# Kernel tuning notes

Measured on AMD Instinct MI355X. Metric: run time of the kernel, lower is better.

Reference implementation:

```python
import jax, jax.numpy as jnp
import numpy as np

B, N_OBJ, OBJ_D = 256, 36, 2048
ATT_D, EMB_D, DEC_D, VOCAB, T = 1024, 1024, 1024, 10000, 20


def setup_inputs() -> dict:
    key = jax.random.key(0)
    ks = jax.random.split(key, 16)
    s = lambda *d: 1.0 / np.sqrt(d[-1])
    inp = {
        'encoder_out': jax.random.normal(ks[0], (B, EMB_D), jnp.float32),
        'objects': jax.random.normal(ks[1], (B, N_OBJ, OBJ_D), jnp.float32),
        'encoded_captions': jax.random.randint(ks[2], (B, T), 0, VOCAB),
        'caption_lengths': jax.random.randint(ks[3], (B, 1), 1, T + 1),
        'emb_table': jax.random.normal(ks[4], (VOCAB, EMB_D), jnp.float32) * 0.02,
        'W_enc_att': jax.random.normal(ks[5], (ATT_D, OBJ_D), jnp.float32) * s(OBJ_D),
        'b_enc_att': jnp.zeros((ATT_D,), jnp.float32),
        'W_dec_att': jax.random.normal(ks[6], (ATT_D, DEC_D), jnp.float32) * s(DEC_D),
        'b_dec_att': jnp.zeros((ATT_D,), jnp.float32),
        'w_full_att': jax.random.normal(ks[7], (1, ATT_D), jnp.float32) * s(ATT_D),
        'b_full_att': jnp.zeros((1,), jnp.float32),
        'W_fbeta': jax.random.normal(ks[8], (OBJ_D, DEC_D), jnp.float32) * s(DEC_D),
        'b_fbeta': jnp.zeros((OBJ_D,), jnp.float32),
        'W_ih': jax.random.normal(ks[9], (4 * DEC_D, EMB_D + OBJ_D), jnp.float32) * s(EMB_D + OBJ_D),
        'W_hh': jax.random.normal(ks[10], (4 * DEC_D, DEC_D), jnp.float32) * s(DEC_D),
        'b_ih': jnp.zeros((4 * DEC_D,), jnp.float32),
        'b_hh': jnp.zeros((4 * DEC_D,), jnp.float32),
        'W_fc': jax.random.normal(ks[11], (VOCAB, DEC_D), jnp.float32) * s(DEC_D),
        'b_fc': jnp.zeros((VOCAB,), jnp.float32),
    }
    return inp


def reference(encoder_out, objects, encoded_captions, caption_lengths,
              emb_table, W_enc_att, b_enc_att, W_dec_att, b_dec_att,
              w_full_att, b_full_att, W_fbeta, b_fbeta,
              W_ih, W_hh, b_ih, b_hh, W_fc, b_fc):
    lengths = caption_lengths[:, 0]
    sort_ind = jnp.argsort(-lengths)  # descending
    lengths = lengths[sort_ind]
    encoder_out = encoder_out[sort_ind]
    objects = objects[sort_ind]
    encoded_captions = encoded_captions[sort_ind]

    embeddings = emb_table[encoded_captions]  # (B, T, E)
    # step t input: encoder_out at t=0, embeddings[:, t-1] afterwards
    step_x = jnp.concatenate([encoder_out[:, None, :], embeddings[:, : T - 1, :]], axis=1)  # (B,T,E)

    att1 = jnp.einsum('bno,ao->bna', objects, W_enc_att) + b_enc_att  # (B,N,A), h-independent

    def step(carry, xs):
        h, c = carry
        x_t, t = xs  # (B,E), scalar
        active = (t < lengths)[:, None]  # (B,1) -- batch_size_t masking (lengths sorted desc)
        att2 = h @ W_dec_att.T + b_dec_att  # (B,A)
        e = (jax.nn.relu(att1 + att2[:, None, :]) @ w_full_att[0] + b_full_att[0])  # (B,N)
        alpha = jax.nn.softmax(e, axis=1)
        awe = jnp.einsum('bn,bno->bo', alpha, objects)  # (B,O)
        gate = jax.nn.sigmoid(h @ W_fbeta.T + b_fbeta)
        awe = gate * awe
        gates = jnp.concatenate([x_t, awe], axis=-1) @ W_ih.T + b_ih + h @ W_hh.T + b_hh
        i, f, g, o = jnp.split(gates, 4, axis=-1)  # torch LSTMCell order
        c_new = jax.nn.sigmoid(f) * c + jax.nn.sigmoid(i) * jnp.tanh(g)
        h_new = jax.nn.sigmoid(o) * jnp.tanh(c_new)
        h = jnp.where(active, h_new, h)
        c = jnp.where(active, c_new, c)
        preds = h_new @ W_fc.T + b_fc  # dropout in eval mode = identity
        preds = jnp.where(active, preds, 0.0)
        alpha = jnp.where(active, alpha, 0.0)
        return (h, c), (preds, alpha)

    h0 = jnp.zeros((B, DEC_D), objects.dtype)
    c0 = jnp.zeros((B, DEC_D), objects.dtype)
    xs = (jnp.swapaxes(step_x, 0, 1), jnp.arange(T))
    _, (preds, alphas) = jax.lax.scan(step, (h0, c0), xs)
    predictions = jnp.swapaxes(preds, 0, 1)  # (B,T,V)
    alphas = jnp.swapaxes(alphas, 0, 1)      # (B,T,N)
    return predictions, encoded_captions, lengths, alphas, sort_ind
```

## Files before the change

kernel.cpp:

```cpp
#include <hip/hip_runtime.h>
#include <hip/hip_bf16.h>
#include <cstdint>
#include <cstddef>

#define BB 256
#define TT 20
#define NOBJ 36
#define OBJD 2048
#define ATTD 1024
#define DECD 1024
#define VOCAB 10000
#define NHC   7168
#define VOCP  10112

typedef unsigned short u16;
typedef __attribute__((ext_vector_type(8))) short short8v;
typedef __attribute__((ext_vector_type(4))) float f32x4;

__device__ inline u16 f2bf(float f) {
    __hip_bfloat16 h = __float2bfloat16(f);
    return *reinterpret_cast<u16*>(&h);
}
__device__ inline float bu(u16 u) {
    union { unsigned int i; float f; } x;
    x.i = ((unsigned int)u) << 16;
    return x.f;
}
__device__ inline float sigf(float x) { return 1.f / (1.f + expf(-x)); }

__device__ inline void gload16(const u16* g, u16* l) {
    __builtin_amdgcn_global_load_lds(
        (const __attribute__((address_space(1))) unsigned int*)g,
        (__attribute__((address_space(3))) unsigned int*)l, 16, 0, 0);
}

__global__ __launch_bounds__(256) void sort_kernel(
    const int* __restrict__ lens, int* __restrict__ sidx, int* __restrict__ slen,
    int* __restrict__ cnt, float* __restrict__ out_len, float* __restrict__ out_sind)
{
    __shared__ int L[BB];
    __shared__ int SL[BB];
    const int i = threadIdx.x;
    const int li = lens[i];
    L[i] = li;
    __syncthreads();
    int r = 0;
    for (int j = 0; j < BB; ++j) {
        const int lj = L[j];
        if (lj > li || (lj == li && j < i)) r++;
    }
    sidx[r] = i;
    slen[r] = li;
    SL[r] = li;
    out_sind[r] = (float)i;
    out_len[r]  = (float)li;
    __syncthreads();
    if (i < TT) {
        int cc = 0;
        for (int b = 0; b < BB; ++b) cc += (SL[b] > i);
        cnt[i] = cc;
    }
}

__global__ __launch_bounds__(256) void meta_kernel(
    const int* __restrict__ caps, const int* __restrict__ sidx,
    float* __restrict__ out_caps)
{
    const int idx = blockIdx.x * 256 + threadIdx.x;
    const int p = idx / TT, t = idx % TT;
    out_caps[idx] = (float)caps[sidx[p] * TT + t];
}

__global__ __launch_bounds__(256) void gather_objs(
    const float* __restrict__ objs, const int* __restrict__ sidx,
    u16* __restrict__ objsb)
{
    const int row = blockIdx.x;
    const int b = row / NOBJ, n = row - b * NOBJ;
    const float* src = objs + ((size_t)sidx[b] * NOBJ + n) * OBJD;
    u16* dst = objsb + (size_t)row * OBJD;
    const int tid = threadIdx.x;
    #pragma unroll
    for (int j = 0; j < 2; ++j) {
        float4 v = ((const float4*)src)[tid + 256 * j];
        ushort4 s;
        s.x = f2bf(v.x); s.y = f2bf(v.y); s.z = f2bf(v.z); s.w = f2bf(v.w);
        ((ushort4*)dst)[tid + 256 * j] = s;
    }
}

__global__ __launch_bounds__(256) void convWhc(
    const float* __restrict__ Wda, const float* __restrict__ bda,
    const float* __restrict__ Wfb, const float* __restrict__ bfb,
    const float* __restrict__ Whh,
    u16* __restrict__ Wb, float* __restrict__ bcat)
{
    const int n = blockIdx.x;
    const int tid = threadIdx.x;
    const float* src;
    float bb = 0.f;
    if (n < 1024)      { src = Wda + (size_t)n * 1024;          bb = bda[n]; }
    else if (n < 3072) { src = Wfb + (size_t)(n - 1024) * 1024; bb = bfb[n - 1024]; }
    else {
        const int loc = n - 3072, q = loc & 3, d = loc >> 2;
        src = Whh + ((size_t)q * 1024 + d) * 1024;
    }
    float4 v = ((const float4*)src)[tid];
    ushort4 s;
    s.x = f2bf(v.x); s.y = f2bf(v.y); s.z = f2bf(v.z); s.w = f2bf(v.w);
    ((ushort4*)(Wb + (size_t)n * 1024))[tid] = s;
    if (tid == 0) bcat[n] = bb;
}

__global__ __launch_bounds__(256) void convWfc(
    const float* __restrict__ Wfc, u16* __restrict__ Wb)
{
    const int n = blockIdx.x;
    const int tid = threadIdx.x;
    ushort4 s;
    if (n < VOCAB) {
        float4 v = ((const float4*)(Wfc + (size_t)n * 1024))[tid];
        s.x = f2bf(v.x); s.y = f2bf(v.y); s.z = f2bf(v.z); s.w = f2bf(v.w);
    } else { s.x = s.y = s.z = s.w = 0; }
    ((ushort4*)(Wb + (size_t)n * 1024))[tid] = s;
}

__global__ __launch_bounds__(256) void convWih(
    const float* __restrict__ Wih, const float* __restrict__ bih,
    const float* __restrict__ bhh, u16* __restrict__ Wb, float* __restrict__ bsum)
{
    const int n = blockIdx.x;
    const int q = n & 3, d = n >> 2;
    const int tid = threadIdx.x;
    const float* src = Wih + ((size_t)q * 1024 + d) * 3072;
    u16* dst = Wb + (size_t)n * 3072;
    #pragma unroll
    for (int j = 0; j < 3; ++j) {
        float4 v = ((const float4*)src)[tid + 256 * j];
        ushort4 s;
        s.x = f2bf(v.x); s.y = f2bf(v.y); s.z = f2bf(v.z); s.w = f2bf(v.w);
        ((ushort4*)dst)[tid + 256 * j] = s;
    }
    if (tid == 0) bsum[n] = bih[q * 1024 + d] + bhh[q * 1024 + d];
}

__global__ __launch_bounds__(256) void convWea(
    const float* __restrict__ Wea, u16* __restrict__ Wb)
{
    const int n = blockIdx.x;
    const int tid = threadIdx.x;
    const float* src = Wea + (size_t)n * OBJD;
    u16* dst = Wb + (size_t)n * OBJD;
    #pragma unroll
    for (int j = 0; j < 2; ++j) {
        float4 v = ((const float4*)src)[tid + 256 * j];
        ushort4 s;
        s.x = f2bf(v.x); s.y = f2bf(v.y); s.z = f2bf(v.z); s.w = f2bf(v.w);
        ((ushort4*)dst)[tid + 256 * j] = s;
    }
}

__global__ __launch_bounds__(256) void embed_kernel(
    const float* __restrict__ enc, const int* __restrict__ caps,
    const float* __restrict__ emb, const int* __restrict__ sidx,
    u16* __restrict__ Xb)
{
    const int blk = blockIdx.x;
    const int t = blk >> 8;
    const int b = blk & 255;
    const int sb = sidx[b];
    const float* src = (t == 0) ? (enc + (size_t)sb * DECD)
                                : (emb + (size_t)caps[sb * TT + (t - 1)] * DECD);
    const int tid = threadIdx.x;
    float4 v = ((const float4*)src)[tid];
    ushort4 s;
    s.x = f2bf(v.x); s.y = f2bf(v.y); s.z = f2bf(v.z); s.w = f2bf(v.w);
    ((ushort4*)(Xb + (size_t)blk * DECD))[tid] = s;
}

__global__ __launch_bounds__(256) void zero_c(float* __restrict__ c)
{
    ((float4*)c)[blockIdx.x * 256 + threadIdx.x] = make_float4(0.f, 0.f, 0.f, 0.f);
}

__global__ __launch_bounds__(256) void hcat0_kernel(
    const float* __restrict__ bcat, float* __restrict__ Hcat)
{
    const int col4 = blockIdx.x * 256 + threadIdx.x;
    const int m = blockIdx.y;
    ((float4*)(Hcat + (size_t)m * NHC))[col4] = ((const float4*)bcat)[col4];
}

__device__ __forceinline__ void gemm_core(u16* SH,
    const u16* __restrict__ A, int lda,
    const u16* __restrict__ B, int ldb,
    int K, int m0, int n0, f32x4 acc[4][4])
{
    u16* AsB = SH;
    u16* BsB = SH + 12288;
    const int tid = threadIdx.x;
    const int lane = tid & 63;
    const int w = tid >> 6;
    const int wr = w >> 1, wc = w & 1;

    const int r0 = (w * 2 + 0) * 16 + (lane >> 2);
    const int r1 = (w * 2 + 1) * 16 + (lane >> 2);
    const int s0 = (lane & 3) ^ ((r0 >> 1) & 3);
    const int s1 = (lane & 3) ^ ((r1 >> 1) & 3);
    const u16* gA0 = A + (size_t)(m0 + r0) * lda + s0 * 8;
    const u16* gA1 = A + (size_t)(m0 + r1) * lda + s1 * 8;
    const u16* gB0 = B + (size_t)(n0 + r0) * ldb + s0 * 8;
    const u16* gB1 = B + (size_t)(n0 + r1) * ldb + s1 * 8;
    const int la0 = (w * 2 + 0) * 512;
    const int la1 = (w * 2 + 1) * 512;

    int ia[4], ib[4];
    #pragma unroll
    for (int mi = 0; mi < 4; ++mi) {
        const int r = wr * 64 + mi * 16 + (lane & 15);
        ia[mi] = r * 32 + (((lane >> 4) ^ ((r >> 1) & 3)) << 3);
    }
    #pragma unroll
    for (int nj = 0; nj < 4; ++nj) {
        const int r = wc * 64 + nj * 16 + (lane & 15);
        ib[nj] = r * 32 + (((lane >> 4) ^ ((r >> 1) & 3)) << 3);
    }

    const int nk = K >> 5;
    #pragma unroll
    for (int p = 0; p < 3; ++p) {
        if (p < nk) {
            const int ko = p * 32;
            gload16(gA0 + ko, AsB + p * 4096 + la0);
            gload16(gA1 + ko, AsB + p * 4096 + la1);
            gload16(gB0 + ko, BsB + p * 4096 + la0);
            gload16(gB1 + ko, BsB + p * 4096 + la1);
        }
    }
    int cur = 0;
    for (int it = 0; it < nk; ++it) {
        const int rem = nk - 1 - it;
        if (rem >= 2)      asm volatile("s_waitcnt vmcnt(8)" ::: "memory");
        else if (rem == 1) asm volatile("s_waitcnt vmcnt(4)" ::: "memory");
        else               asm volatile("s_waitcnt vmcnt(0)" ::: "memory");
        __builtin_amdgcn_s_barrier();
        const u16* Asc = AsB + cur * 4096;
        const u16* Bsc = BsB + cur * 4096;
        short8v av[4], bv[4];
        #pragma unroll
        for (int mi = 0; mi < 4; ++mi) av[mi] = *(const short8v*)&Asc[ia[mi]];
        #pragma unroll
        for (int nj = 0; nj < 4; ++nj) bv[nj] = *(const short8v*)&Bsc[ib[nj]];
        __builtin_amdgcn_s_setprio(1);
        #pragma unroll
        for (int mi = 0; mi < 4; ++mi)
            #pragma unroll
            for (int nj = 0; nj < 4; ++nj)
                acc[mi][nj] = __builtin_amdgcn_mfma_f32_16x16x32_bf16(
                    av[mi], bv[nj], acc[mi][nj], 0, 0, 0);
        __builtin_amdgcn_s_setprio(0);
        __builtin_amdgcn_s_barrier();
        if (it + 3 < nk) {
            const int ko = (it + 3) * 32;
            gload16(gA0 + ko, AsB + cur * 4096 + la0);
            gload16(gA1 + ko, AsB + cur * 4096 + la1);
            gload16(gB0 + ko, BsB + cur * 4096 + la0);
            gload16(gB1 + ko, BsB + cur * 4096 + la1);
        }
        cur = (cur == 2) ? 0 : cur + 1;
    }
}

__global__ __launch_bounds__(256) void gemm128(
    const u16* __restrict__ A, int lda,
    const u16* __restrict__ B, int ldb,
    const float* __restrict__ bias,
    float* __restrict__ Cf, u16* __restrict__ Cb, int ldc,
    int Nreal, int K, int pairM, const int* __restrict__ cntp)
{
    __shared__ __align__(16) u16 SH[24576];
    int nIdx, mIdx;
    if (pairM) { nIdx = blockIdx.x >> 1; mIdx = blockIdx.x & 1; }
    else       { nIdx = blockIdx.x;      mIdx = blockIdx.y; }
    const int m0 = mIdx * 128;
    const int n0 = nIdx * 128;
    if (cntp && m0 >= *cntp) return;

    f32x4 acc[4][4];
    #pragma unroll
    for (int i = 0; i < 4; ++i)
        #pragma unroll
        for (int j = 0; j < 4; ++j) acc[i][j] = (f32x4){0.f, 0.f, 0.f, 0.f};
    gemm_core(SH, A, lda, B, ldb, K, m0, n0, acc);

    const int lane = threadIdx.x & 63, w = threadIdx.x >> 6;
    const int wr = w >> 1, wc = w & 1;
    #pragma unroll
    for (int mi = 0; mi < 4; ++mi) {
        const int mbase = m0 + wr * 64 + mi * 16 + ((lane >> 4) << 2);
        #pragma unroll
        for (int nj = 0; nj < 4; ++nj) {
            const int n = n0 + wc * 64 + nj * 16 + (lane & 15);
            if (n >= Nreal) continue;
            const float bval = bias ? bias[n] : 0.f;
            #pragma unroll
            for (int r = 0; r < 4; ++r) {
                const int m = mbase + r;
                const float v = acc[mi][nj][r] + bval;
                if (Cb) Cb[(size_t)m * ldc + n] = f2bf(v);
                else    Cf[(size_t)m * ldc + n] = v;
            }
        }
    }
}

__global__ __launch_bounds__(256) void g2l_kernel(
    const u16* __restrict__ aweb, const u16* __restrict__ Wihb,
    const u16* __restrict__ Gxb_t, const float* __restrict__ Hcat,
    float* __restrict__ c, u16* __restrict__ hb_t,
    const int* __restrict__ cntp)
{
    __shared__ __align__(16) u16 SH[24576];
    const int bid = blockIdx.x, tid = threadIdx.x;
    const int m0 = (bid & 1) * 128, n0 = (bid >> 1) * 128;
    const int act = *cntp;
    if (m0 >= act) return;

    f32x4 acc[4][4];
    #pragma unroll
    for (int i = 0; i < 4; ++i)
        #pragma unroll
        for (int j = 0; j < 4; ++j) acc[i][j] = (f32x4){0.f, 0.f, 0.f, 0.f};
    gemm_core(SH, aweb, 2048, Wihb + 1024, 3072, 2048, m0, n0, acc);

    const int lane = tid & 63, w = tid >> 6;
    const int wr = w >> 1, wc = w & 1;
    float* patch = (float*)SH;
    #pragma unroll
    for (int half = 0; half < 2; ++half) {
        __syncthreads();
        if (wr == half) {
            #pragma unroll
            for (int mi = 0; mi < 4; ++mi) {
                const int rbase = mi * 16 + ((lane >> 4) << 2);
                #pragma unroll
                for (int nj = 0; nj < 4; ++nj) {
                    const int col = wc * 64 + nj * 16 + (lane & 15);
                    #pragma unroll
                    for (int r = 0; r < 4; ++r)
                        patch[(rbase + r) * 128 + col] = acc[mi][nj][r];
                }
            }
        }
        __syncthreads();
        const int h0 = half * 64;
        #pragma unroll
        for (int p8 = 0; p8 < 8; ++p8) {
            const int idx = p8 * 256 + tid;
            const int row = idx >> 5, dl = idx & 31;
            const int b = m0 + h0 + row;
            if (b >= act) continue;
            const int d = (n0 >> 2) + dl;
            const float* pr = patch + row * 128 + dl * 4;
            float gi = pr[0], gf = pr[1], gg = pr[2], go = pr[3];
            const ushort4 xv = *(const ushort4*)(Gxb_t + (size_t)b * 4096 + n0 + dl * 4);
            gi += bu(xv.x); gf += bu(xv.y); gg += bu(xv.z); go += bu(xv.w);
            const float4 hv = *(const float4*)(Hcat + (size_t)b * NHC + 3072 + n0 + dl * 4);
            gi += hv.x; gf += hv.y; gg += hv.z; go += hv.w;
            float* cp = c + (size_t)b * 1024 + d;
            const float cn = sigf(gf) * cp[0] + sigf(gi) * tanhf(gg);
            const float hn = sigf(go) * tanhf(cn);
            cp[0] = cn;
            hb_t[(size_t)b * 1024 + d] = f2bf(hn);
        }
    }
}

__global__ __launch_bounds__(256) void preds_gemm(
    const u16* __restrict__ hball, const u16* __restrict__ Wfcb,
    const float* __restrict__ bfc, const int* __restrict__ cnt,
    float* __restrict__ outP)
{
    __shared__ __align__(16) u16 SH[24576];
    const int m0 = blockIdx.y * 128;
    const int n0 = blockIdx.x * 128;
    const int t = m0 >> 8;
    const int act = cnt[t];
    const int bbase = m0 & 255;

    f32x4 acc[4][4];
    #pragma unroll
    for (int i = 0; i < 4; ++i)
        #pragma unroll
        for (int j = 0; j < 4; ++j) acc[i][j] = (f32x4){0.f, 0.f, 0.f, 0.f};
    if (bbase < act)
        gemm_core(SH, hball, 1024, Wfcb, 1024, 1024, m0, n0, acc);

    const int lane = threadIdx.x & 63, w = threadIdx.x >> 6;
    const int wr = w >> 1, wc = w & 1;
    #pragma unroll
    for (int mi = 0; mi < 4; ++mi) {
        const int mbase = bbase + wr * 64 + mi * 16 + ((lane >> 4) << 2);
        #pragma unroll
        for (int nj = 0; nj < 4; ++nj) {
            const int n = n0 + wc * 64 + nj * 16 + (lane & 15);
            if (n >= VOCAB) continue;
            const float bval = bfc[n];
            #pragma unroll
            for (int r = 0; r < 4; ++r) {
                const int b = mbase + r;
                outP[((size_t)b * TT + t) * VOCAB + n] =
                    (b < act) ? (acc[mi][nj][r] + bval) : 0.f;
            }
        }
    }
}

__global__ __launch_bounds__(256) void attn_kernel(
    const u16* __restrict__ att1b, const float* __restrict__ Hcat,
    const u16* __restrict__ objsb,
    const float* __restrict__ wfa, const float* __restrict__ bfa,
    const int* __restrict__ slen, int t,
    float* __restrict__ out_alph, u16* __restrict__ aweb)
{
    const int b = blockIdx.x, z = blockIdx.y, tid = threadIdx.x;
    const bool active = t < slen[b];
    if (!active) {
        if (z == 0 && tid < NOBJ)
            out_alph[((size_t)b * TT + t) * NOBJ + tid] = 0.f;
        return;
    }
    __shared__ float wred[4][40];
    __shared__ float es[40];
    __shared__ float alph[40];
    const int lane = tid & 63, w = tid >> 6;
    const float* hrow = Hcat + (size_t)b * NHC;
    const float4 h4 = ((const float4*)hrow)[tid];
    const float4 w4 = ((const float4*)wfa)[tid];
    const u16* a1base = att1b + (size_t)b * NOBJ * ATTD;

    float ep[NOBJ];
    #pragma unroll
    for (int n = 0; n < NOBJ; ++n) {
        ushort4 a4 = ((const ushort4*)(a1base + (size_t)n * ATTD))[tid];
        const float v0 = fmaxf(bu(a4.x) + h4.x, 0.f);
        const float v1 = fmaxf(bu(a4.y) + h4.y, 0.f);
        const float v2 = fmaxf(bu(a4.z) + h4.z, 0.f);
        const float v3 = fmaxf(bu(a4.w) + h4.w, 0.f);
        ep[n] = v0 * w4.x + v1 * w4.y + v2 * w4.z + v3 * w4.w;
    }
    #pragma unroll
    for (int n = 0; n < NOBJ; ++n) {
        float p = ep[n];
        #pragma unroll
        for (int off = 32; off > 0; off >>= 1) p += __shfl_down(p, off, 64);
        if (lane == 0) wred[w][n] = p;
    }
    __syncthreads();
    if (tid < NOBJ)
        es[tid] = wred[0][tid] + wred[1][tid] + wred[2][tid] + wred[3][tid] + bfa[0];
    __syncthreads();
    if (tid < 64) {
        float mv = (tid < NOBJ) ? es[tid] : -1e30f;
        #pragma unroll
        for (int off = 32; off > 0; off >>= 1) mv = fmaxf(mv, __shfl_xor(mv, off, 64));
        float e = (tid < NOBJ) ? expf(es[tid] - mv) : 0.f;
        float s = e;
        #pragma unroll
        for (int off = 32; off > 0; off >>= 1) s += __shfl_xor(s, off, 64);
        if (tid < NOBJ) alph[tid] = e / s;
    }
    __syncthreads();
    if (z == 0 && tid < NOBJ)
        out_alph[((size_t)b * TT + t) * NOBJ + tid] = alph[tid];

    float acc[4] = {0.f, 0.f, 0.f, 0.f};
    const u16* ob = objsb + (size_t)b * NOBJ * OBJD + z * 1024 + tid * 4;
    #pragma unroll 4
    for (int n = 0; n < NOBJ; ++n) {
        const ushort4 ov = *(const ushort4*)(ob + (size_t)n * OBJD);
        const float al = alph[n];
        acc[0] = fmaf(al, bu(ov.x), acc[0]);
        acc[1] = fmaf(al, bu(ov.y), acc[1]);
        acc[2] = fmaf(al, bu(ov.z), acc[2]);
        acc[3] = fmaf(al, bu(ov.w), acc[3]);
    }
    const float4 g0 = *(const float4*)(hrow + 1024 + z * 1024 + tid * 4);
    ushort4 st;
    st.x = f2bf(acc[0] * sigf(g0.x));
    st.y = f2bf(acc[1] * sigf(g0.y));
    st.z = f2bf(acc[2] * sigf(g0.z));
    st.w = f2bf(acc[3] * sigf(g0.w));
    *(ushort4*)&aweb[(size_t)b * 2048 + z * 1024 + tid * 4] = st;
}

extern "C" void kernel_launch(void* const* d_in, const int* in_sizes, int n_in,
                              void* d_out, int out_size, void* d_ws, size_t ws_size,
                              hipStream_t stream)
{
    const float* enc  = (const float*)d_in[0];
    const float* objs = (const float*)d_in[1];
    const int*   caps = (const int*)d_in[2];
    const int*   clen = (const int*)d_in[3];
    const float* emb  = (const float*)d_in[4];
    const float* Wea  = (const float*)d_in[5];
    const float* bea  = (const float*)d_in[6];
    const float* Wda  = (const float*)d_in[7];
    const float* bda  = (const float*)d_in[8];
    const float* wfa  = (const float*)d_in[9];
    const float* bfa  = (const float*)d_in[10];
    const float* Wfb  = (const float*)d_in[11];
    const float* bfb  = (const float*)d_in[12];
    const float* Wih  = (const float*)d_in[13];
    const float* Whh  = (const float*)d_in[14];
    const float* bih  = (const float*)d_in[15];
    const float* bhh  = (const float*)d_in[16];
    const float* Wfc  = (const float*)d_in[17];
    const float* bfc  = (const float*)d_in[18];

    float* outP     = (float*)d_out;
    float* out_caps = outP + (size_t)BB * TT * VOCAB;
    float* out_len  = out_caps + BB * TT;
    float* out_alph = out_len + BB;
    float* out_sind = out_alph + (size_t)BB * TT * NOBJ;

    char* wp = (char*)d_ws;
    auto alloc = [&](size_t bytes) -> void* {
        void* r = (void*)wp;
        wp += (bytes + 255) & ~(size_t)255;
        return r;
    };
    int*   sidx  = (int*)alloc(BB * 4);
    int*   slen  = (int*)alloc(BB * 4);
    int*   cnt   = (int*)alloc(32 * 4);
    u16*   objsb = (u16*)alloc((size_t)BB * NOBJ * OBJD * 2);
    u16*   Whcb  = (u16*)alloc((size_t)NHC * 1024 * 2);
    float* bcat  = (float*)alloc(NHC * 4);
    u16*   Wfcb  = (u16*)alloc((size_t)VOCP * 1024 * 2);
    u16*   Wihb  = (u16*)alloc((size_t)4096 * 3072 * 2);
    float* bsum  = (float*)alloc(4096 * 4);
    u16*   Weab  = (u16*)alloc((size_t)1024 * OBJD * 2);
    u16*   att1b = (u16*)alloc((size_t)BB * NOBJ * ATTD * 2);
    u16*   Xb    = (u16*)alloc((size_t)TT * BB * DECD * 2);
    u16*   Gxb   = (u16*)alloc((size_t)TT * BB * 4096 * 2);
    float* Hcat  = (float*)alloc((size_t)BB * NHC * 4);
    u16*   aweb  = (u16*)alloc((size_t)BB * 2048 * 2);
    u16*   hball = (u16*)alloc((size_t)TT * BB * DECD * 2);
    float* c     = (float*)alloc((size_t)BB * DECD * 4);
    (void)ws_size; (void)in_sizes; (void)n_in; (void)out_size;

    sort_kernel<<<1, 256, 0, stream>>>(clen, sidx, slen, cnt, out_len, out_sind);
    meta_kernel<<<20, 256, 0, stream>>>(caps, sidx, out_caps);
    gather_objs<<<BB * NOBJ, 256, 0, stream>>>(objs, sidx, objsb);
    convWhc<<<NHC, 256, 0, stream>>>(Wda, bda, Wfb, bfb, Whh, Whcb, bcat);
    convWfc<<<VOCP, 256, 0, stream>>>(Wfc, Wfcb);
    convWih<<<4096, 256, 0, stream>>>(Wih, bih, bhh, Wihb, bsum);
    convWea<<<1024, 256, 0, stream>>>(Wea, Weab);
    embed_kernel<<<TT * BB, 256, 0, stream>>>(enc, caps, emb, sidx, Xb);
    zero_c<<<256, 256, 0, stream>>>(c);
    hcat0_kernel<<<dim3(7, 256), 256, 0, stream>>>(bcat, Hcat);

    gemm128<<<dim3(8, 72), 256, 0, stream>>>(
        objsb, OBJD, Weab, OBJD, bea, nullptr, att1b, ATTD,
        ATTD, OBJD, 0, nullptr);

    gemm128<<<dim3(32, 40), 256, 0, stream>>>(
        Xb, DECD, Wihb, 3072, bsum, nullptr, Gxb, 4096,
        4096, DECD, 0, nullptr);

    for (int t = 0; t < TT; ++t) {
        attn_kernel<<<dim3(BB, 2), 256, 0, stream>>>(
            att1b, Hcat, objsb, wfa, bfa, slen, t, out_alph, aweb);
        g2l_kernel<<<64, 256, 0, stream>>>(
            aweb, Wihb, Gxb + (size_t)t * BB * 4096, Hcat, c,
            hball + (size_t)t * BB * DECD, cnt + t);
        if (t < TT - 1)
            gemm128<<<112, 256, 0, stream>>>(
                hball + (size_t)t * BB * DECD, DECD, Whcb, DECD, bcat,
                Hcat, nullptr, NHC, NHC, DECD, 1, cnt + t);
    }

    preds_gemm<<<dim3(VOCP / 128, 40), 256, 0, stream>>>(
        hball, Wfcb, bfc, cnt, outP);
}
```

Baseline: 1.728 ms.

## Overlap W_hh projection with attention and remap preds GEMM block order

Each step's hidden-state GEMM is split. Only the attention/gate columns (first 3072) are computed right after the LSTM cell, and the W_hh recurrent columns are computed by extra blocks inside the next step's attention kernel, so they run concurrently with the attention work. The attention kernel now uses one block per batch row with 8-wide loads instead of two half-blocks. The preds GEMM uses a 1D grid that sweeps pairs of M tiles across all N tiles for better weight reuse in cache. This cuts the critical path per step, but the combined kernel gets heavier shared-memory use and mixed block types. The W_hh part also drops the bias add, on the assumption that the bias is already folded in elsewhere.

```diff
diff --git a/kernel.cpp b/kernel.cpp
--- a/kernel.cpp
+++ b/kernel.cpp
@@ -312,6 +312,118 @@
             }
         }
     }
+}
+
+__global__ __launch_bounds__(256) void attnwhh_kernel(
+    const u16* __restrict__ att1b, float* __restrict__ Hcat,
+    const u16* __restrict__ objsb,
+    const float* __restrict__ wfa, const float* __restrict__ bfa,
+    const int* __restrict__ slen, int t,
+    float* __restrict__ out_alph, u16* __restrict__ aweb,
+    const u16* __restrict__ hb_prev, const u16* __restrict__ Whcb,
+    const int* __restrict__ cnt_prev)
+{
+    __shared__ __align__(16) u16 SH[24576];
+    __shared__ float wred[4][40];
+    __shared__ float es[40];
+    __shared__ float alph[40];
+    const int tid = threadIdx.x;
+
+    if (blockIdx.x >= 256) {
+        if (t == 0) return;
+        const int j = blockIdx.x - 256;
+        const int n0 = (j >> 1) * 128;
+        const int m0 = (j & 1) * 128;
+        if (m0 >= *cnt_prev) return;
+        f32x4 acc[4][4];
+        #pragma unroll
+        for (int i = 0; i < 4; ++i)
+            #pragma unroll
+            for (int jj = 0; jj < 4; ++jj) acc[i][jj] = (f32x4){0.f, 0.f, 0.f, 0.f};
+        gemm_core(SH, hb_prev, DECD, Whcb + (size_t)3072 * 1024, DECD,
+                  DECD, m0, n0, acc);
+        const int lane = tid & 63, w = tid >> 6;
+        const int wr = w >> 1, wc = w & 1;
+        #pragma unroll
+        for (int mi = 0; mi < 4; ++mi) {
+            const int mbase = m0 + wr * 64 + mi * 16 + ((lane >> 4) << 2);
+            #pragma unroll
+            for (int nj = 0; nj < 4; ++nj) {
+                const int n = n0 + wc * 64 + nj * 16 + (lane & 15);
+                #pragma unroll
+                for (int r = 0; r < 4; ++r)
+                    Hcat[(size_t)(mbase + r) * NHC + 3072 + n] = acc[mi][nj][r];
+            }
+        }
+        return;
+    }
+
+    const int b = blockIdx.x;
+    const bool active = t < slen[b];
+    if (!active) {
+        if (tid < NOBJ)
+            out_alph[((size_t)b * TT + t) * NOBJ + tid] = 0.f;
+        return;
+    }
+    const int lane = tid & 63, w = tid >> 6;
+    const float* hrow = Hcat + (size_t)b * NHC;
+    const float4 h4 = ((const float4*)hrow)[tid];
+    const float4 w4 = ((const float4*)wfa)[tid];
+    const u16* a1base = att1b + (size_t)b * NOBJ * ATTD;
+
+    float ep[NOBJ];
+    #pragma unroll
+    for (int n = 0; n < NOBJ; ++n) {
+        ushort4 a4 = ((const ushort4*)(a1base + (size_t)n * ATTD))[tid];
+        const float v0 = fmaxf(bu(a4.x) + h4.x, 0.f);
+        const float v1 = fmaxf(bu(a4.y) + h4.y, 0.f);
+        const float v2 = fmaxf(bu(a4.z) + h4.z, 0.f);
+        const float v3 = fmaxf(bu(a4.w) + h4.w, 0.f);
+        ep[n] = v0 * w4.x + v1 * w4.y + v2 * w4.z + v3 * w4.w;
+    }
+    #pragma unroll
+    for (int n = 0; n < NOBJ; ++n) {
+        float p = ep[n];
+        #pragma unroll
+        for (int off = 32; off > 0; off >>= 1) p += __shfl_down(p, off, 64);
+        if (lane == 0) wred[w][n] = p;
+    }
+    __syncthreads();
+    if (tid < NOBJ)
+        es[tid] = wred[0][tid] + wred[1][tid] + wred[2][tid] + wred[3][tid] + bfa[0];
+    __syncthreads();
+    if (tid < 64) {
+        float mv = (tid < NOBJ) ? es[tid] : -1e30f;
+        #pragma unroll
+        for (int off = 32; off > 0; off >>= 1) mv = fmaxf(mv, __shfl_xor(mv, off, 64));
+        float e = (tid < NOBJ) ? expf(es[tid] - mv) : 0.f;
+        float s = e;
+        #pragma unroll
+        for (int off = 32; off > 0; off >>= 1) s += __shfl_xor(s, off, 64);
+        if (tid < NOBJ) alph[tid] = e / s;
+    }
+    __syncthreads();
+    if (tid < NOBJ)
+        out_alph[((size_t)b * TT + t) * NOBJ + tid] = alph[tid];
+
+    float acc8[8] = {0.f, 0.f, 0.f, 0.f, 0.f, 0.f, 0.f, 0.f};
+    const u16* ob = objsb + (size_t)b * NOBJ * OBJD + tid * 8;
+    #pragma unroll 4
+    for (int n = 0; n < NOBJ; ++n) {
+        const short8v ov = *(const short8v*)(ob + (size_t)n * OBJD);
+        const float al = alph[n];
+        #pragma unroll
+        for (int j = 0; j < 8; ++j) acc8[j] = fmaf(al, bu((u16)ov[j]), acc8[j]);
+    }
+    const float* gp = hrow + 1024 + tid * 8;
+    const float4 g0 = *(const float4*)gp;
+    const float4 g1 = *(const float4*)(gp + 4);
+    const float gt[8] = {sigf(g0.x), sigf(g0.y), sigf(g0.z), sigf(g0.w),
+                         sigf(g1.x), sigf(g1.y), sigf(g1.z), sigf(g1.w)};
+    short8v st;
+    #pragma unroll
+    for (int j = 0; j < 8; ++j) st[j] = (short)f2bf(acc8[j] * gt[j]);
+    *(short8v*)&aweb[(size_t)b * 2048 + tid * 8] = st;
 }
 
 __global__ __launch_bounds__(256) void g2l_kernel(
@@ -382,8 +494,11 @@
     float* __restrict__ outP)
 {
     __shared__ __align__(16) u16 SH[24576];
-    const int m0 = blockIdx.y * 128;
-    const int n0 = blockIdx.x * 128;
+    const int bid = blockIdx.x;
+    const int sweep = bid / 158;
+    const int rem = bid - sweep * 158;
+    const int n0 = (rem >> 1) * 128;
+    const int m0 = (sweep * 2 + (rem & 1)) * 128;
     const int t = m0 >> 8;
     const int act = cnt[t];
     const int bbase = m0 & 255;
@@ -414,84 +529,6 @@
             }
         }
     }
-}
-
-__global__ __launch_bounds__(256) void attn_kernel(
-    const u16* __restrict__ att1b, const float* __restrict__ Hcat,
-    const u16* __restrict__ objsb,
-    const float* __restrict__ wfa, const float* __restrict__ bfa,
-    const int* __restrict__ slen, int t,
-    float* __restrict__ out_alph, u16* __restrict__ aweb)
-{
-    const int b = blockIdx.x, z = blockIdx.y, tid = threadIdx.x;
-    const bool active = t < slen[b];
-    if (!active) {
-        if (z == 0 && tid < NOBJ)
-            out_alph[((size_t)b * TT + t) * NOBJ + tid] = 0.f;
-        return;
-    }
-    __shared__ float wred[4][40];
-    __shared__ float es[40];
-    __shared__ float alph[40];
-    const int lane = tid & 63, w = tid >> 6;
-    const float* hrow = Hcat + (size_t)b * NHC;
-    const float4 h4 = ((const float4*)hrow)[tid];
-    const float4 w4 = ((const float4*)wfa)[tid];
-    const u16* a1base = att1b + (size_t)b * NOBJ * ATTD;
-
-    float ep[NOBJ];
-    #pragma unroll
-    for (int n = 0; n < NOBJ; ++n) {
-        ushort4 a4 = ((const ushort4*)(a1base + (size_t)n * ATTD))[tid];
-        const float v0 = fmaxf(bu(a4.x) + h4.x, 0.f);
-        const float v1 = fmaxf(bu(a4.y) + h4.y, 0.f);
-        const float v2 = fmaxf(bu(a4.z) + h4.z, 0.f);
-        const float v3 = fmaxf(bu(a4.w) + h4.w, 0.f);
-        ep[n] = v0 * w4.x + v1 * w4.y + v2 * w4.z + v3 * w4.w;
-    }
-    #pragma unroll
-    for (int n = 0; n < NOBJ; ++n) {
-        float p = ep[n];
-        #pragma unroll
-        for (int off = 32; off > 0; off >>= 1) p += __shfl_down(p, off, 64);
-        if (lane == 0) wred[w][n] = p;
-    }
-    __syncthreads();
-    if (tid < NOBJ)
-        es[tid] = wred[0][tid] + wred[1][tid] + wred[2][tid] + wred[3][tid] + bfa[0];
-    __syncthreads();
-    if (tid < 64) {
-        float mv = (tid < NOBJ) ? es[tid] : -1e30f;
-        #pragma unroll
-        for (int off = 32; off > 0; off >>= 1) mv = fmaxf(mv, __shfl_xor(mv, off, 64));
-        float e = (tid < NOBJ) ? expf(es[tid] - mv) : 0.f;
-        float s = e;
-        #pragma unroll
-        for (int off = 32; off > 0; off >>= 1) s += __shfl_xor(s, off, 64);
-        if (tid < NOBJ) alph[tid] = e / s;
-    }
-    __syncthreads();
-    if (z == 0 && tid < NOBJ)
-        out_alph[((size_t)b * TT + t) * NOBJ + tid] = alph[tid];
-
-    float acc[4] = {0.f, 0.f, 0.f, 0.f};
-    const u16* ob = objsb + (size_t)b * NOBJ * OBJD + z * 1024 + tid * 4;
-    #pragma unroll 4
-    for (int n = 0; n < NOBJ; ++n) {
-        const ushort4 ov = *(const ushort4*)(ob + (size_t)n * OBJD);
-        const float al = alph[n];
-        acc[0] = fmaf(al, bu(ov.x), acc[0]);
-        acc[1] = fmaf(al, bu(ov.y), acc[1]);
-        acc[2] = fmaf(al, bu(ov.z), acc[2]);
-        acc[3] = fmaf(al, bu(ov.w), acc[3]);
-    }
-    const float4 g0 = *(const float4*)(hrow + 1024 + z * 1024 + tid * 4);
-    ushort4 st;
-    st.x = f2bf(acc[0] * sigf(g0.x));
-    st.y = f2bf(acc[1] * sigf(g0.y));
-    st.z = f2bf(acc[2] * sigf(g0.z));
-    st.w = f2bf(acc[3] * sigf(g0.w));
-    *(ushort4*)&aweb[(size_t)b * 2048 + z * 1024 + tid * 4] = st;
 }
 
 extern "C" void kernel_launch(void* const* d_in, const int* in_sizes, int n_in,
@@ -569,17 +606,18 @@
         4096, DECD, 0, nullptr);
 
     for (int t = 0; t < TT; ++t) {
-        attn_kernel<<<dim3(BB, 2), 256, 0, stream>>>(
-            att1b, Hcat, objsb, wfa, bfa, slen, t, out_alph, aweb);
+        attnwhh_kernel<<<320, 256, 0, stream>>>(
+            att1b, Hcat, objsb, wfa, bfa, slen, t, out_alph, aweb,
+            hball + (size_t)(t > 0 ? t - 1 : 0) * BB * DECD, Whcb,
+            cnt + (t > 0 ? t - 1 : 0));
         g2l_kernel<<<64, 256, 0, stream>>>(
             aweb, Wihb, Gxb + (size_t)t * BB * 4096, Hcat, c,
             hball + (size_t)t * BB * DECD, cnt + t);
         if (t < TT - 1)
-            gemm128<<<112, 256, 0, stream>>>(
+            gemm128<<<48, 256, 0, stream>>>(
                 hball + (size_t)t * BB * DECD, DECD, Whcb, DECD, bcat,
-                Hcat, nullptr, NHC, NHC, DECD, 1, cnt + t);
-    }
-
-    preds_gemm<<<dim3(VOCP / 128, 40), 256, 0, stream>>>(
-        hball, Wfcb, bfc, cnt, outP);
-}
+                Hcat, nullptr, NHC, 3072, DECD, 1, cnt + t);
+    }
+
+    preds_gemm<<<3160, 256, 0, stream>>>(hball, Wfcb, bfc, cnt, outP);
+}
```

New measurement: 1.827 ms. 5.7% more time.

## Deepen GEMM prefetch pipeline for recurrent kernels and remap preds grid

Applied to the files above, without the earlier changes.

Templates the GEMM core on pipeline depth, using an 8-stage global-to-LDS prefetch for the per-step recurrent GEMMs (g2l and the hidden-state GEMM) and keeping 3 stages elsewhere. These kernels launch only 64-112 blocks, so deeper in-flight loads are meant to hide memory latency. The preds GEMM becomes a 1D grid of 3200 blocks with a swizzled block-to-tile mapping, and the vocab padding grows to 10240 so the tiles divide evenly. The larger LDS footprint (128KB per block) limits each CU to one block, which matters little at these grid sizes.

```diff
diff --git a/kernel.cpp b/kernel.cpp
--- a/kernel.cpp
+++ b/kernel.cpp
@@ -11,7 +11,7 @@
 #define DECD 1024
 #define VOCAB 10000
 #define NHC   7168
-#define VOCP  10112
+#define VOCP  10240
 
 typedef unsigned short u16;
 typedef __attribute__((ext_vector_type(8))) short short8v;
@@ -32,6 +32,21 @@
     __builtin_amdgcn_global_load_lds(
         (const __attribute__((address_space(1))) unsigned int*)g,
         (__attribute__((address_space(3))) unsigned int*)l, 16, 0, 0);
+}
+
+template<int DEPTH>
+__device__ __forceinline__ void wait_tiles(int rem) {
+    const int r = rem < DEPTH - 1 ? rem : DEPTH - 1;
+    switch (r) {
+        case 0: asm volatile("s_waitcnt vmcnt(0)" ::: "memory"); break;
+        case 1: asm volatile("s_waitcnt vmcnt(4)" ::: "memory"); break;
+        case 2: asm volatile("s_waitcnt vmcnt(8)" ::: "memory"); break;
+        case 3: asm volatile("s_waitcnt vmcnt(12)" ::: "memory"); break;
+        case 4: asm volatile("s_waitcnt vmcnt(16)" ::: "memory"); break;
+        case 5: asm volatile("s_waitcnt vmcnt(20)" ::: "memory"); break;
+        case 6: asm volatile("s_waitcnt vmcnt(24)" ::: "memory"); break;
+        default: asm volatile("s_waitcnt vmcnt(28)" ::: "memory"); break;
+    }
 }
 
 __global__ __launch_bounds__(256) void sort_kernel(
@@ -191,13 +206,14 @@
     ((float4*)(Hcat + (size_t)m * NHC))[col4] = ((const float4*)bcat)[col4];
 }
 
+template<int DEPTH>
 __device__ __forceinline__ void gemm_core(u16* SH,
     const u16* __restrict__ A, int lda,
     const u16* __restrict__ B, int ldb,
     int K, int m0, int n0, f32x4 acc[4][4])
 {
     u16* AsB = SH;
-    u16* BsB = SH + 12288;
+    u16* BsB = SH + DEPTH * 4096;
     const int tid = threadIdx.x;
     const int lane = tid & 63;
     const int w = tid >> 6;
@@ -228,7 +244,7 @@
 
     const int nk = K >> 5;
     #pragma unroll
-    for (int p = 0; p < 3; ++p) {
+    for (int p = 0; p < DEPTH; ++p) {
         if (p < nk) {
             const int ko = p * 32;
             gload16(gA0 + ko, AsB + p * 4096 + la0);
@@ -239,10 +255,7 @@
     }
     int cur = 0;
     for (int it = 0; it < nk; ++it) {
-        const int rem = nk - 1 - it;
-        if (rem >= 2)      asm volatile("s_waitcnt vmcnt(8)" ::: "memory");
-        else if (rem == 1) asm volatile("s_waitcnt vmcnt(4)" ::: "memory");
-        else               asm volatile("s_waitcnt vmcnt(0)" ::: "memory");
+        wait_tiles<DEPTH>(nk - 1 - it);
         __builtin_amdgcn_s_barrier();
         const u16* Asc = AsB + cur * 4096;
         const u16* Bsc = BsB + cur * 4096;
@@ -260,17 +273,18 @@
                     av[mi], bv[nj], acc[mi][nj], 0, 0, 0);
         __builtin_amdgcn_s_setprio(0);
         __builtin_amdgcn_s_barrier();
-        if (it + 3 < nk) {
-            const int ko = (it + 3) * 32;
+        if (it + DEPTH < nk) {
+            const int ko = (it + DEPTH) * 32;
             gload16(gA0 + ko, AsB + cur * 4096 + la0);
             gload16(gA1 + ko, AsB + cur * 4096 + la1);
             gload16(gB0 + ko, BsB + cur * 4096 + la0);
             gload16(gB1 + ko, BsB + cur * 4096 + la1);
         }
-        cur = (cur == 2) ? 0 : cur + 1;
-    }
-}
-
+        cur = (cur == DEPTH - 1) ? 0 : cur + 1;
+    }
+}
+
+template<int DEPTH>
 __global__ __launch_bounds__(256) void gemm128(
     const u16* __restrict__ A, int lda,
     const u16* __restrict__ B, int ldb,
@@ -278,7 +292,7 @@
     float* __restrict__ Cf, u16* __restrict__ Cb, int ldc,
     int Nreal, int K, int pairM, const int* __restrict__ cntp)
 {
-    __shared__ __align__(16) u16 SH[24576];
+    __shared__ __align__(16) u16 SH[2 * DEPTH * 4096];
     int nIdx, mIdx;
     if (pairM) { nIdx = blockIdx.x >> 1; mIdx = blockIdx.x & 1; }
     else       { nIdx = blockIdx.x;      mIdx = blockIdx.y; }
@@ -291,7 +305,7 @@
     for (int i = 0; i < 4; ++i)
         #pragma unroll
         for (int j = 0; j < 4; ++j) acc[i][j] = (f32x4){0.f, 0.f, 0.f, 0.f};
-    gemm_core(SH, A, lda, B, ldb, K, m0, n0, acc);
+    gemm_core<DEPTH>(SH, A, lda, B, ldb, K, m0, n0, acc);
 
     const int lane = threadIdx.x & 63, w = threadIdx.x >> 6;
     const int wr = w >> 1, wc = w & 1;
@@ -320,7 +334,7 @@
     float* __restrict__ c, u16* __restrict__ hb_t,
     const int* __restrict__ cntp)
 {
-    __shared__ __align__(16) u16 SH[24576];
+    __shared__ __align__(16) u16 SH[2 * 8 * 4096];
     const int bid = blockIdx.x, tid = threadIdx.x;
     const int m0 = (bid & 1) * 128, n0 = (bid >> 1) * 128;
     const int act = *cntp;
@@ -331,7 +345,7 @@
     for (int i = 0; i < 4; ++i)
         #pragma unroll
         for (int j = 0; j < 4; ++j) acc[i][j] = (f32x4){0.f, 0.f, 0.f, 0.f};
-    gemm_core(SH, aweb, 2048, Wihb + 1024, 3072, 2048, m0, n0, acc);
+    gemm_core<8>(SH, aweb, 2048, Wihb + 1024, 3072, 2048, m0, n0, acc);
 
     const int lane = tid & 63, w = tid >> 6;
     const int wr = w >> 1, wc = w & 1;
@@ -381,9 +395,12 @@
     const float* __restrict__ bfc, const int* __restrict__ cnt,
     float* __restrict__ outP)
 {
-    __shared__ __align__(16) u16 SH[24576];
-    const int m0 = blockIdx.y * 128;
-    const int n0 = blockIdx.x * 128;
+    __shared__ __align__(16) u16 SH[2 * 3 * 4096];
+    const int bid = blockIdx.x;
+    const int x = bid & 7;
+    const int j = bid >> 3;
+    const int n0 = (x * 10 + (j % 10)) * 128;
+    const int m0 = (j / 10) * 128;
     const int t = m0 >> 8;
     const int act = cnt[t];
     const int bbase = m0 & 255;
@@ -392,9 +409,9 @@
     #pragma unroll
     for (int i = 0; i < 4; ++i)
         #pragma unroll
-        for (int j = 0; j < 4; ++j) acc[i][j] = (f32x4){0.f, 0.f, 0.f, 0.f};
+        for (int jj = 0; jj < 4; ++jj) acc[i][jj] = (f32x4){0.f, 0.f, 0.f, 0.f};
     if (bbase < act)
-        gemm_core(SH, hball, 1024, Wfcb, 1024, 1024, m0, n0, acc);
+        gemm_core<3>(SH, hball, 1024, Wfcb, 1024, 1024, m0, n0, acc);
 
     const int lane = threadIdx.x & 63, w = threadIdx.x >> 6;
     const int wr = w >> 1, wc = w & 1;
@@ -560,11 +577,11 @@
     zero_c<<<256, 256, 0, stream>>>(c);
     hcat0_kernel<<<dim3(7, 256), 256, 0, stream>>>(bcat, Hcat);
 
-    gemm128<<<dim3(8, 72), 256, 0, stream>>>(
+    gemm128<3><<<dim3(8, 72), 256, 0, stream>>>(
         objsb, OBJD, Weab, OBJD, bea, nullptr, att1b, ATTD,
         ATTD, OBJD, 0, nullptr);
 
-    gemm128<<<dim3(32, 40), 256, 0, stream>>>(
+    gemm128<3><<<dim3(32, 40), 256, 0, stream>>>(
         Xb, DECD, Wihb, 3072, bsum, nullptr, Gxb, 4096,
         4096, DECD, 0, nullptr);
 
@@ -575,11 +592,10 @@
             aweb, Wihb, Gxb + (size_t)t * BB * 4096, Hcat, c,
             hball + (size_t)t * BB * DECD, cnt + t);
         if (t < TT - 1)
-            gemm128<<<112, 256, 0, stream>>>(
+            gemm128<8><<<112, 256, 0, stream>>>(
                 hball + (size_t)t * BB * DECD, DECD, Whcb, DECD, bcat,
                 Hcat, nullptr, NHC, NHC, DECD, 1, cnt + t);
     }
 
-    preds_gemm<<<dim3(VOCP / 128, 40), 256, 0, stream>>>(
-        hball, Wfcb, bfc, cnt, outP);
-}
+    preds_gemm<<<3200, 256, 0, stream>>>(hball, Wfcb, bfc, cnt, outP);
+}
```

Result: slower. 1.907 ms (+10.4%).

## Fuse per-step output projection into the recurrent hidden-state GEMM

Applied to the files above, without the earlier changes.

Concatenates the vocabulary projection weights with the attention/gate/W_hh weights so that each timestep runs one GEMM over h producing both the next-step Hcat terms and that step's predictions. The separate end-of-loop preds GEMM and the hball history buffer are removed. The 128x128 tiles are block-swizzled so M-pairs share B tiles. The intent is to fill the GPU better during the small per-step GEMMs, which had only 112 blocks, by giving them 272 blocks. In exchange, the predictions work now sits on the serial per-step critical path, and the final step runs a GEMM that was previously skipped.

```diff
diff --git a/kernel.cpp b/kernel.cpp
--- a/kernel.cpp
+++ b/kernel.cpp
@@ -11,7 +11,9 @@
 #define DECD 1024
 #define VOCAB 10000
 #define NHC   7168
-#define VOCP  10112
+#define NBIG  17168
+#define NBIGP 17408
+#define NSPLIT 7168
 
 typedef unsigned short u16;
 typedef __attribute__((ext_vector_type(8))) short short8v;
@@ -89,40 +91,31 @@
     }
 }
 
-__global__ __launch_bounds__(256) void convWhc(
+__global__ __launch_bounds__(256) void convWbig(
     const float* __restrict__ Wda, const float* __restrict__ bda,
     const float* __restrict__ Wfb, const float* __restrict__ bfb,
     const float* __restrict__ Whh,
+    const float* __restrict__ Wfc, const float* __restrict__ bfc,
     u16* __restrict__ Wb, float* __restrict__ bcat)
 {
     const int n = blockIdx.x;
     const int tid = threadIdx.x;
-    const float* src;
+    const float* src = nullptr;
     float bb = 0.f;
     if (n < 1024)      { src = Wda + (size_t)n * 1024;          bb = bda[n]; }
     else if (n < 3072) { src = Wfb + (size_t)(n - 1024) * 1024; bb = bfb[n - 1024]; }
-    else {
+    else if (n < 7168) {
         const int loc = n - 3072, q = loc & 3, d = loc >> 2;
         src = Whh + ((size_t)q * 1024 + d) * 1024;
     }
-    float4 v = ((const float4*)src)[tid];
+    else if (n < NBIG) { src = Wfc + (size_t)(n - NHC) * 1024;  bb = bfc[n - NHC]; }
     ushort4 s;
-    s.x = f2bf(v.x); s.y = f2bf(v.y); s.z = f2bf(v.z); s.w = f2bf(v.w);
-    ((ushort4*)(Wb + (size_t)n * 1024))[tid] = s;
-    if (tid == 0) bcat[n] = bb;
-}
-
-__global__ __launch_bounds__(256) void convWfc(
-    const float* __restrict__ Wfc, u16* __restrict__ Wb)
-{
-    const int n = blockIdx.x;
-    const int tid = threadIdx.x;
-    ushort4 s;
-    if (n < VOCAB) {
-        float4 v = ((const float4*)(Wfc + (size_t)n * 1024))[tid];
+    if (src) {
+        float4 v = ((const float4*)src)[tid];
         s.x = f2bf(v.x); s.y = f2bf(v.y); s.z = f2bf(v.z); s.w = f2bf(v.w);
     } else { s.x = s.y = s.z = s.w = 0; }
     ((ushort4*)(Wb + (size_t)n * 1024))[tid] = s;
+    if (tid == 0) bcat[n] = bb;
 }
 
 __global__ __launch_bounds__(256) void convWih(
@@ -276,15 +269,11 @@
     const u16* __restrict__ B, int ldb,
     const float* __restrict__ bias,
     float* __restrict__ Cf, u16* __restrict__ Cb, int ldc,
-    int Nreal, int K, int pairM, const int* __restrict__ cntp)
+    int Nreal, int K)
 {
     __shared__ __align__(16) u16 SH[24576];
-    int nIdx, mIdx;
-    if (pairM) { nIdx = blockIdx.x >> 1; mIdx = blockIdx.x & 1; }
-    else       { nIdx = blockIdx.x;      mIdx = blockIdx.y; }
-    const int m0 = mIdx * 128;
-    const int n0 = nIdx * 128;
-    if (cntp && m0 >= *cntp) return;
+    const int m0 = blockIdx.y * 128;
+    const int n0 = blockIdx.x * 128;
 
     f32x4 acc[4][4];
     #pragma unroll
@@ -309,6 +298,51 @@
                 const float v = acc[mi][nj][r] + bval;
                 if (Cb) Cb[(size_t)m * ldc + n] = f2bf(v);
                 else    Cf[(size_t)m * ldc + n] = v;
+            }
+        }
+    }
+}
+
+__global__ __launch_bounds__(256) void big_gemm(
+    const u16* __restrict__ hb, const u16* __restrict__ Wbigb,
+    const float* __restrict__ bcat, const int* __restrict__ cntp,
+    float* __restrict__ Hcat, float* __restrict__ outP_t)
+{
+    __shared__ __align__(16) u16 SH[24576];
+    const int bid = blockIdx.x;
+    const int n0 = ((bid >> 4) * 8 + (bid & 7)) * 128;
+    const int m0 = ((bid >> 3) & 1) * 128;
+    const int act = *cntp;
+    const bool live = (m0 < act);
+
+    f32x4 acc[4][4];
+    #pragma unroll
+    for (int i = 0; i < 4; ++i)
+        #pragma unroll
+        for (int j = 0; j < 4; ++j) acc[i][j] = (f32x4){0.f, 0.f, 0.f, 0.f};
+    if (live)
+        gemm_core(SH, hb, DECD, Wbigb, DECD, DECD, m0, n0, acc);
+
+    const int lane = threadIdx.x & 63, w = threadIdx.x >> 6;
+    const int wr = w >> 1, wc = w & 1;
+    #pragma unroll
+    for (int mi = 0; mi < 4; ++mi) {
+        const int mbase = m0 + wr * 64 + mi * 16 + ((lane >> 4) << 2);
+        #pragma unroll
+        for (int nj = 0; nj < 4; ++nj) {
+            const int n = n0 + wc * 64 + nj * 16 + (lane & 15);
+            if (n >= NBIG) continue;
+            const float bval = bcat[n];
+            #pragma unroll
+            for (int r = 0; r < 4; ++r) {
+                const int m = mbase + r;
+                const float v = acc[mi][nj][r] + bval;
+                if (n < NSPLIT) {
+                    if (live) Hcat[(size_t)m * NHC + n] = v;
+                } else {
+                    outP_t[(size_t)m * (TT * VOCAB) + (n - NSPLIT)] =
+                        (m < act) ? v : 0.f;
+                }
             }
         }
     }
@@ -372,46 +406,6 @@
             const float hn = sigf(go) * tanhf(cn);
             cp[0] = cn;
             hb_t[(size_t)b * 1024 + d] = f2bf(hn);
-        }
-    }
-}
-
-__global__ __launch_bounds__(256) void preds_gemm(
-    const u16* __restrict__ hball, const u16* __restrict__ Wfcb,
-    const float* __restrict__ bfc, const int* __restrict__ cnt,
-    float* __restrict__ outP)
-{
-    __shared__ __align__(16) u16 SH[24576];
-    const int m0 = blockIdx.y * 128;
-    const int n0 = blockIdx.x * 128;
-    const int t = m0 >> 8;
-    const int act = cnt[t];
-    const int bbase = m0 & 255;
-
-    f32x4 acc[4][4];
-    #pragma unroll
-    for (int i = 0; i < 4; ++i)
-        #pragma unroll
-        for (int j = 0; j < 4; ++j) acc[i][j] = (f32x4){0.f, 0.f, 0.f, 0.f};
-    if (bbase < act)
-        gemm_core(SH, hball, 1024, Wfcb, 1024, 1024, m0, n0, acc);
-
-    const int lane = threadIdx.x & 63, w = threadIdx.x >> 6;
-    const int wr = w >> 1, wc = w & 1;
-    #pragma unroll
-    for (int mi = 0; mi < 4; ++mi) {
-        const int mbase = bbase + wr * 64 + mi * 16 + ((lane >> 4) << 2);
-        #pragma unroll
-        for (int nj = 0; nj < 4; ++nj) {
-            const int n = n0 + wc * 64 + nj * 16 + (lane & 15);
-            if (n >= VOCAB) continue;
-            const float bval = bfc[n];
-            #pragma unroll
-            for (int r = 0; r < 4; ++r) {
-                const int b = mbase + r;
-                outP[((size_t)b * TT + t) * VOCAB + n] =
-                    (b < act) ? (acc[mi][nj][r] + bval) : 0.f;
-            }
         }
     }
 }
@@ -534,9 +528,8 @@
     int*   slen  = (int*)alloc(BB * 4);
     int*   cnt   = (int*)alloc(32 * 4);
     u16*   objsb = (u16*)alloc((size_t)BB * NOBJ * OBJD * 2);
-    u16*   Whcb  = (u16*)alloc((size_t)NHC * 1024 * 2);
-    float* bcat  = (float*)alloc(NHC * 4);
-    u16*   Wfcb  = (u16*)alloc((size_t)VOCP * 1024 * 2);
+    u16*   Wbigb = (u16*)alloc((size_t)NBIGP * 1024 * 2);
+    float* bcat  = (float*)alloc(NBIGP * 4);
     u16*   Wihb  = (u16*)alloc((size_t)4096 * 3072 * 2);
     float* bsum  = (float*)alloc(4096 * 4);
     u16*   Weab  = (u16*)alloc((size_t)1024 * OBJD * 2);
@@ -545,15 +538,14 @@
     u16*   Gxb   = (u16*)alloc((size_t)TT * BB * 4096 * 2);
     float* Hcat  = (float*)alloc((size_t)BB * NHC * 4);
     u16*   aweb  = (u16*)alloc((size_t)BB * 2048 * 2);
-    u16*   hball = (u16*)alloc((size_t)TT * BB * DECD * 2);
+    u16*   hb    = (u16*)alloc((size_t)BB * DECD * 2);
     float* c     = (float*)alloc((size_t)BB * DECD * 4);
     (void)ws_size; (void)in_sizes; (void)n_in; (void)out_size;
 
     sort_kernel<<<1, 256, 0, stream>>>(clen, sidx, slen, cnt, out_len, out_sind);
     meta_kernel<<<20, 256, 0, stream>>>(caps, sidx, out_caps);
     gather_objs<<<BB * NOBJ, 256, 0, stream>>>(objs, sidx, objsb);
-    convWhc<<<NHC, 256, 0, stream>>>(Wda, bda, Wfb, bfb, Whh, Whcb, bcat);
-    convWfc<<<VOCP, 256, 0, stream>>>(Wfc, Wfcb);
+    convWbig<<<NBIGP, 256, 0, stream>>>(Wda, bda, Wfb, bfb, Whh, Wfc, bfc, Wbigb, bcat);
     convWih<<<4096, 256, 0, stream>>>(Wih, bih, bhh, Wihb, bsum);
     convWea<<<1024, 256, 0, stream>>>(Wea, Weab);
     embed_kernel<<<TT * BB, 256, 0, stream>>>(enc, caps, emb, sidx, Xb);
@@ -561,25 +553,17 @@
     hcat0_kernel<<<dim3(7, 256), 256, 0, stream>>>(bcat, Hcat);
 
     gemm128<<<dim3(8, 72), 256, 0, stream>>>(
-        objsb, OBJD, Weab, OBJD, bea, nullptr, att1b, ATTD,
-        ATTD, OBJD, 0, nullptr);
+        objsb, OBJD, Weab, OBJD, bea, nullptr, att1b, ATTD, ATTD, OBJD);
 
     gemm128<<<dim3(32, 40), 256, 0, stream>>>(
-        Xb, DECD, Wihb, 3072, bsum, nullptr, Gxb, 4096,
-        4096, DECD, 0, nullptr);
+        Xb, DECD, Wihb, 3072, bsum, nullptr, Gxb, 4096, 4096, DECD);
 
     for (int t = 0; t < TT; ++t) {
         attn_kernel<<<dim3(BB, 2), 256, 0, stream>>>(
             att1b, Hcat, objsb, wfa, bfa, slen, t, out_alph, aweb);
         g2l_kernel<<<64, 256, 0, stream>>>(
-            aweb, Wihb, Gxb + (size_t)t * BB * 4096, Hcat, c,
-            hball + (size_t)t * BB * DECD, cnt + t);
-        if (t < TT - 1)
-            gemm128<<<112, 256, 0, stream>>>(
-                hball + (size_t)t * BB * DECD, DECD, Whcb, DECD, bcat,
-                Hcat, nullptr, NHC, NHC, DECD, 1, cnt + t);
-    }
-
-    preds_gemm<<<dim3(VOCP / 128, 40), 256, 0, stream>>>(
-        hball, Wfcb, bfc, cnt, outP);
-}
+            aweb, Wihb, Gxb + (size_t)t * BB * 4096, Hcat, c, hb, cnt + t);
+        big_gemm<<<272, 256, 0, stream>>>(
+            hb, Wbigb, bcat, cnt + t, Hcat, outP + (size_t)t * VOCAB);
+    }
+}
```

Result: no change. 1.761 ms (+1.9%).
